# Optimization experiments

Hardware: AMD Instinct MI355X
Metric: run time of the kernel (lower is better)

The kernel has to match this reference:

```python
import jax, jax.numpy as jnp
import numpy as np

B, K, N, D, H, DOUT = 16, 8, 196, 768, 3072, 768


def setup_inputs() -> dict:
    key = jax.random.key(0)
    ks = jax.random.split(key, 5)
    scale_w1 = 1.0 / np.sqrt(D)
    scale_w2 = 1.0 / np.sqrt(H)
    return {
        "slots": jax.random.normal(ks[0], (B, K, D), dtype=jnp.float32),
        "pos_embed": jax.random.normal(ks[1], (N, D), dtype=jnp.float32) * 0.02,
        "map_alpha": jax.random.normal(ks[2], (N, DOUT), dtype=jnp.float32) * 0.02,
        "W1": jax.random.normal(ks[3], (D, H), dtype=jnp.float32) * scale_w1,
        "b1": jnp.zeros((H,), dtype=jnp.float32),
        "W2": jax.random.normal(ks[4], (H, DOUT), dtype=jnp.float32) * scale_w2,
        "b2": jnp.zeros((DOUT,), dtype=jnp.float32),
    }


def reference(slots, pos_embed, map_alpha, W1, b1, W2, b2):
    b, k, d = slots.shape
    n = pos_embed.shape[0]
    # broadcast slots over patches and add positional embedding: (B,K,N,D)
    tokens = slots[:, :, None, :] + pos_embed[None, None, :, :]
    # 2-layer MLP with ReLU
    h = jax.nn.relu(jnp.einsum('bknd,dh->bknh', tokens, W1) + b1)
    y_k = jnp.einsum('bknh,ho->bkno', h, W2) + b2  # (B,K,N,DOUT)
    # softmax over K of map_alpha expanded over (B,K); identical across K -> uniform 1/K,
    # computed explicitly for faithfulness to the original module
    m_k = jax.nn.softmax(jnp.broadcast_to(map_alpha[None, None, :, :], (b, k, n, map_alpha.shape[1])), axis=1)
    y = jnp.einsum('bknd,bknd->bnd', y_k, m_k)
    return y
```

## Files before the change

### kernel.cpp

```cpp
#include <hip/hip_runtime.h>
#include <hip/hip_bf16.h>
#include <stdint.h>


typedef __attribute__((ext_vector_type(8))) short bf16x8;
typedef __attribute__((ext_vector_type(4))) float f32x4;

#define AS1 __attribute__((address_space(1)))
#define AS3 __attribute__((address_space(3)))

#define WAIT_VM(N) asm volatile("s_waitcnt vmcnt(" #N ")" ::: "memory")
#define BAR()      asm volatile("s_barrier" ::: "memory")
#define BAR_LDS()  asm volatile("s_waitcnt lgkmcnt(0)\ns_barrier" ::: "memory")

static __device__ __forceinline__ void gld_lds16(const void* g, void* l) {
    __builtin_amdgcn_global_load_lds((const AS1 unsigned int*)g,
                                     (AS3 unsigned int*)l, 16, 0, 0);
}

static __device__ __forceinline__ unsigned short f2bf(float f) {
    union { float f; unsigned int u; } v; v.f = f;
    unsigned int u = v.u;
    return (unsigned short)((u + 0x7fffu + ((u >> 16) & 1u)) >> 16);
}

static __device__ __forceinline__ void conv_tiled(const float* __restrict__ W,
                                                  unsigned short* __restrict__ Wt,
                                                  int Kd, int Rd, int idx) {
    int r  = idx % Rd;
    int kc = idx / Rd;
    unsigned int po[4];
    #pragma unroll
    for (int j = 0; j < 4; ++j) {
        unsigned short lo = f2bf(W[(size_t)(kc * 8 + 2 * j) * Rd + r]);
        unsigned short hi = f2bf(W[(size_t)(kc * 8 + 2 * j + 1) * Rd + r]);
        po[j] = (unsigned int)lo | ((unsigned int)hi << 16);
    }
    size_t dst = ((size_t)(r >> 6) * (Kd >> 6) + (kc >> 3)) * 4096
               + (size_t)((kc & 7) * 64 + (r & 63)) * 8;
    *(uint4*)(Wt + dst) = make_uint4(po[0], po[1], po[2], po[3]);
}

__global__ void k_prep(const float* __restrict__ W1, unsigned short* __restrict__ W1t,
                       const float* __restrict__ W2, unsigned short* __restrict__ W2t,
                       const float* __restrict__ S, const float* __restrict__ P,
                       unsigned short* __restrict__ A1) {
    int idx = blockIdx.x * blockDim.x + threadIdx.x;
    const int C1n = 96 * 3072;
    const int C2n = 384 * 768;
    const int PKn = 96 * 384;
    if (idx < C1n) {
        conv_tiled(W1, W1t, 768, 3072, idx);
    } else if (idx < C1n + C2n) {
        conv_tiled(W2, W2t, 3072, 768, idx - C1n);
    } else if (idx < C1n + C2n + PKn) {
        int t = idx - C1n - C2n;
        int r  = t % 384;
        int kc = t / 384;
        uint4 o = make_uint4(0u, 0u, 0u, 0u);
        if (r < 324) {
            const float* src = (r < 128) ? (S + (size_t)r * 768 + kc * 8)
                                         : (P + (size_t)(r - 128) * 768 + kc * 8);
            float4 a = *(const float4*)(src);
            float4 b = *(const float4*)(src + 4);
            o.x = (unsigned int)f2bf(a.x) | ((unsigned int)f2bf(a.y) << 16);
            o.y = (unsigned int)f2bf(a.z) | ((unsigned int)f2bf(a.w) << 16);
            o.z = (unsigned int)f2bf(b.x) | ((unsigned int)f2bf(b.y) << 16);
            o.w = (unsigned int)f2bf(b.z) | ((unsigned int)f2bf(b.w) << 16);
        }
        size_t dst = ((size_t)(r >> 6) * 12 + (kc >> 3)) * 4096
                   + (size_t)((kc & 7) * 64 + (r & 63)) * 8;
        *(uint4*)(A1 + dst) = o;
    }
}

__global__ void k_hbar(const float* __restrict__ C1, const float* __restrict__ b1,
                       unsigned short* __restrict__ Hb) {
    const int lane = threadIdx.x & 63;
    const int wv   = threadIdx.x >> 6;
    const int hc   = blockIdx.y * 4 + wv;
    const int h0   = hc * 8;
    const int bn   = blockIdx.x * 64 + lane;
    const int b    = bn / 196;
    const int n    = bn - b * 196;
    const float* prow = C1 + (size_t)(128 + n) * 3072 + h0;
    float4 pA = *(const float4*)(prow);
    float4 pB = *(const float4*)(prow + 4);
    float4 bA = *(const float4*)(b1 + h0);
    float4 bB = *(const float4*)(b1 + h0 + 4);
    float pb[8] = { pA.x + bA.x, pA.y + bA.y, pA.z + bA.z, pA.w + bA.w,
                    pB.x + bB.x, pB.y + bB.y, pB.z + bB.z, pB.w + bB.w };
    float acc[8] = {};
    #pragma unroll
    for (int k = 0; k < 8; ++k) {
        const float* srow = C1 + (size_t)(b * 8 + k) * 3072 + h0;
        float4 sA_ = *(const float4*)(srow);
        float4 sB_ = *(const float4*)(srow + 4);
        acc[0] += fmaxf(sA_.x + pb[0], 0.f);
        acc[1] += fmaxf(sA_.y + pb[1], 0.f);
        acc[2] += fmaxf(sA_.z + pb[2], 0.f);
        acc[3] += fmaxf(sA_.w + pb[3], 0.f);
        acc[4] += fmaxf(sB_.x + pb[4], 0.f);
        acc[5] += fmaxf(sB_.y + pb[5], 0.f);
        acc[6] += fmaxf(sB_.z + pb[6], 0.f);
        acc[7] += fmaxf(sB_.w + pb[7], 0.f);
    }
    unsigned int w0 = (unsigned int)f2bf(acc[0] * 0.125f) | ((unsigned int)f2bf(acc[1] * 0.125f) << 16);
    unsigned int w1 = (unsigned int)f2bf(acc[2] * 0.125f) | ((unsigned int)f2bf(acc[3] * 0.125f) << 16);
    unsigned int w2 = (unsigned int)f2bf(acc[4] * 0.125f) | ((unsigned int)f2bf(acc[5] * 0.125f) << 16);
    unsigned int w3 = (unsigned int)f2bf(acc[6] * 0.125f) | ((unsigned int)f2bf(acc[7] * 0.125f) << 16);
    size_t dst = ((size_t)blockIdx.x * 48 + (hc >> 3)) * 4096
               + (size_t)((hc & 7) * 64 + lane) * 8;
    *(uint4*)(Hb + dst) = make_uint4(w0, w1, w2, w3);
}

__launch_bounds__(256)
__global__ void gemm_tiled(const unsigned short* __restrict__ A,
                           const unsigned short* __restrict__ Bt,
                           const float* __restrict__ bias,
                           float* __restrict__ C,
                           int Mstore, int Nd, int KT) {
    __shared__ unsigned short smem[2 * 8192];

    const int tid  = threadIdx.x;
    const int lane = tid & 63;
    const int wave = tid >> 6;
    const int wm   = wave >> 1;
    const int wn   = wave & 1;
    const int q    = lane >> 4;
    const int l16  = lane & 15;

    const unsigned short* Abase = A  + (size_t)blockIdx.y * KT * 4096;
    const unsigned short* Bbase = Bt + (size_t)blockIdx.x * KT * 4096;

    f32x4 acc[2][2] = {};

    const int offA0 = ((q * 64) + wm * 32 + l16) * 8;
    const int offB0 = ((q * 64) + wn * 32 + l16) * 8;

    {
        #pragma unroll
        for (int it = 0; it < 2; ++it) {
            int c = it * 256 + tid;
            gld_lds16(Abase + (size_t)c * 8, smem + c * 8);
        }
        #pragma unroll
        for (int it = 0; it < 2; ++it) {
            int c = it * 256 + tid;
            gld_lds16(Bbase + (size_t)c * 8, smem + 4096 + c * 8);
        }
    }

    auto step = [&](const unsigned short* sA, const unsigned short* sB,
                    unsigned short* dA, unsigned short* dB, int i) {
        const bool pf = (i + 1 < KT);
        if (pf) {
            const unsigned short* Ag = Abase + (size_t)(i + 1) * 4096;
            const unsigned short* Bg = Bbase + (size_t)(i + 1) * 4096;
            #pragma unroll
            for (int it = 0; it < 2; ++it) {
                int c = it * 256 + tid;
                gld_lds16(Ag + (size_t)c * 8, dA + c * 8);
            }
            #pragma unroll
            for (int it = 0; it < 2; ++it) {
                int c = it * 256 + tid;
                gld_lds16(Bg + (size_t)c * 8, dB + c * 8);
            }
            WAIT_VM(4);
        } else {
            WAIT_VM(0);
        }
        BAR();
        #pragma unroll
        for (int ks = 0; ks < 2; ++ks) {
            const int ko = ks * 4 * 64 * 8;
            bf16x8 af[2], bfr[2];
            af[0]  = *(const bf16x8*)(sA + offA0 + ko);
            af[1]  = *(const bf16x8*)(sA + offA0 + ko + 16 * 8);
            bfr[0] = *(const bf16x8*)(sB + offB0 + ko);
            bfr[1] = *(const bf16x8*)(sB + offB0 + ko + 16 * 8);
            #pragma unroll
            for (int ii = 0; ii < 2; ++ii)
                #pragma unroll
                for (int jj = 0; jj < 2; ++jj)
                    acc[ii][jj] = __builtin_amdgcn_mfma_f32_16x16x32_bf16(
                        af[ii], bfr[jj], acc[ii][jj], 0, 0, 0);
        }
        if (pf) BAR_LDS();
    };

    for (int i = 0; i < KT; i += 2) {
        step(smem,        smem + 4096, smem + 8192, smem + 12288, i);
        step(smem + 8192, smem + 12288, smem,       smem + 4096,  i + 1);
    }

    const int row0 = blockIdx.y * 64 + wm * 32;
    const int col0 = blockIdx.x * 64 + wn * 32;
    #pragma unroll
    for (int ii = 0; ii < 2; ++ii) {
        #pragma unroll
        for (int jj = 0; jj < 2; ++jj) {
            int col = col0 + jj * 16 + l16;
            float bv = bias ? bias[col] : 0.f;
            #pragma unroll
            for (int r = 0; r < 4; ++r) {
                int row = row0 + ii * 16 + q * 4 + r;
                if (row < Mstore) C[(size_t)row * Nd + col] = acc[ii][jj][r] + bv;
            }
        }
    }
}

extern "C" void kernel_launch(void* const* d_in, const int* in_sizes, int n_in,
                              void* d_out, int out_size, void* d_ws, size_t ws_size,
                              hipStream_t stream) {
    const float* slots  = (const float*)d_in[0];
    const float* pos    = (const float*)d_in[1];
    const float* W1     = (const float*)d_in[3];
    const float* b1     = (const float*)d_in[4];
    const float* W2     = (const float*)d_in[5];
    const float* b2     = (const float*)d_in[6];
    float* out = (float*)d_out;

    size_t off = 0;
    auto alloc = [&](size_t bytes) {
        void* p = (char*)d_ws + off;
        off += (bytes + 255) & ~(size_t)255;
        return p;
    };
    unsigned short* W1t = (unsigned short*)alloc((size_t)3072 * 768 * 2);
    unsigned short* W2t = (unsigned short*)alloc((size_t)768 * 3072 * 2);
    unsigned short* A1  = (unsigned short*)alloc((size_t)384 * 768 * 2);
    float*          C1  = (float*)alloc((size_t)324 * 3072 * 4);
    unsigned short* Hb  = (unsigned short*)alloc((size_t)3136 * 3072 * 2);

    const int total = 96 * 3072 + 384 * 768 + 96 * 384;
    k_prep<<<(total + 255) / 256, 256, 0, stream>>>(W1, W1t, W2, W2t, slots, pos, A1);
    gemm_tiled<<<dim3(48, 6), 256, 0, stream>>>(A1, W1t, nullptr, C1, 324, 3072, 12);
    k_hbar<<<dim3(49, 96), 256, 0, stream>>>(C1, b1, Hb);
    gemm_tiled<<<dim3(12, 49), 256, 0, stream>>>(Hb, W2t, b2, out, 3136, 768, 48);
}
```

Baseline: 138.5 us.

## Widen GEMM tile to 64x128 and split-K over two blocks with atomic accumulation

The GEMM kernel now computes a 64x128 output tile per block, with each wave holding a 32x64 accumulator, so each A fragment is reused across more B columns. K is split across two blocks via blockIdx.z, and partial sums are accumulated with float atomicAdd. The prep kernel now zero-fills C1 and pre-initializes the output with b2 so the atomics can accumulate onto it. This trades fewer A loads and better per-wave MFMA density for atomic write traffic, extra initialization writes, and more LDS per block.

```diff
diff --git a/kernel.cpp b/kernel.cpp
--- a/kernel.cpp
+++ b/kernel.cpp
@@ -44,19 +44,22 @@
 __global__ void k_prep(const float* __restrict__ W1, unsigned short* __restrict__ W1t,
                        const float* __restrict__ W2, unsigned short* __restrict__ W2t,
                        const float* __restrict__ S, const float* __restrict__ P,
-                       unsigned short* __restrict__ A1) {
+                       unsigned short* __restrict__ A1,
+                       float* __restrict__ C1, const float* __restrict__ b2,
+                       float* __restrict__ out) {
     int idx = blockIdx.x * blockDim.x + threadIdx.x;
-    const int C1n = 96 * 3072;
-    const int C2n = 384 * 768;
-    const int PKn = 96 * 384;
-    if (idx < C1n) {
-        conv_tiled(W1, W1t, 768, 3072, idx);
-    } else if (idx < C1n + C2n) {
-        conv_tiled(W2, W2t, 3072, 768, idx - C1n);
-    } else if (idx < C1n + C2n + PKn) {
-        int t = idx - C1n - C2n;
-        int r  = t % 384;
-        int kc = t / 384;
+    const int T1 = 96 * 3072;
+    const int T2 = 384 * 768;
+    const int T3 = 96 * 384;
+    const int T4 = 384 * 3072 / 4;
+    const int T5 = 3136 * 768 / 4;
+    if (idx < T1) { conv_tiled(W1, W1t, 768, 3072, idx); return; }
+    idx -= T1;
+    if (idx < T2) { conv_tiled(W2, W2t, 3072, 768, idx); return; }
+    idx -= T2;
+    if (idx < T3) {
+        int r  = idx % 384;
+        int kc = idx / 384;
         uint4 o = make_uint4(0u, 0u, 0u, 0u);
         if (r < 324) {
             const float* src = (r < 128) ? (S + (size_t)r * 768 + kc * 8)
@@ -71,6 +74,15 @@
         size_t dst = ((size_t)(r >> 6) * 12 + (kc >> 3)) * 4096
                    + (size_t)((kc & 7) * 64 + (r & 63)) * 8;
         *(uint4*)(A1 + dst) = o;
+        return;
+    }
+    idx -= T3;
+    if (idx < T4) { *(float4*)(C1 + (size_t)idx * 4) = make_float4(0.f, 0.f, 0.f, 0.f); return; }
+    idx -= T4;
+    if (idx < T5) {
+        int m = idx / 192;
+        int r = idx - m * 192;
+        *(float4*)(out + (size_t)m * 768 + r * 4) = *(const float4*)(b2 + r * 4);
     }
 }
 
@@ -117,10 +129,9 @@
 __launch_bounds__(256)
 __global__ void gemm_tiled(const unsigned short* __restrict__ A,
                            const unsigned short* __restrict__ Bt,
-                           const float* __restrict__ bias,
                            float* __restrict__ C,
-                           int Mstore, int Nd, int KT) {
-    __shared__ unsigned short smem[2 * 8192];
+                           int Mstore, int Nd, int aKT, int bKT, int ktPer) {
+    __shared__ unsigned short smem[2 * 12288];
 
     const int tid  = threadIdx.x;
     const int lane = tid & 63;
@@ -129,84 +140,77 @@
     const int wn   = wave & 1;
     const int q    = lane >> 4;
     const int l16  = lane & 15;
-
-    const unsigned short* Abase = A  + (size_t)blockIdx.y * KT * 4096;
-    const unsigned short* Bbase = Bt + (size_t)blockIdx.x * KT * 4096;
-
-    f32x4 acc[2][2] = {};
-
-    const int offA0 = ((q * 64) + wm * 32 + l16) * 8;
-    const int offB0 = ((q * 64) + wn * 32 + l16) * 8;
-
-    {
-        #pragma unroll
-        for (int it = 0; it < 2; ++it) {
-            int c = it * 256 + tid;
-            gld_lds16(Abase + (size_t)c * 8, smem + c * 8);
-        }
-        #pragma unroll
-        for (int it = 0; it < 2; ++it) {
-            int c = it * 256 + tid;
-            gld_lds16(Bbase + (size_t)c * 8, smem + 4096 + c * 8);
-        }
-    }
-
-    auto step = [&](const unsigned short* sA, const unsigned short* sB,
-                    unsigned short* dA, unsigned short* dB, int i) {
-        const bool pf = (i + 1 < KT);
-        if (pf) {
-            const unsigned short* Ag = Abase + (size_t)(i + 1) * 4096;
-            const unsigned short* Bg = Bbase + (size_t)(i + 1) * 4096;
-            #pragma unroll
-            for (int it = 0; it < 2; ++it) {
-                int c = it * 256 + tid;
-                gld_lds16(Ag + (size_t)c * 8, dA + c * 8);
-            }
-            #pragma unroll
-            for (int it = 0; it < 2; ++it) {
-                int c = it * 256 + tid;
-                gld_lds16(Bg + (size_t)c * 8, dB + c * 8);
-            }
-            WAIT_VM(4);
-        } else {
-            WAIT_VM(0);
-        }
-        BAR();
+    const int nt   = blockIdx.x;
+    const int rt   = blockIdx.y;
+    const int kt0  = blockIdx.z * ktPer;
+
+    const unsigned short* Ab = A  + ((size_t)rt * aKT + kt0) * 4096;
+    const unsigned short* B0 = Bt + ((size_t)(2 * nt)     * bKT + kt0) * 4096;
+    const unsigned short* B1 = Bt + ((size_t)(2 * nt + 1) * bKT + kt0) * 4096;
+
+    f32x4 acc[2][4] = {};
+
+    auto stage = [&](int i, unsigned short* dst) {
+        const unsigned short* Ag  = Ab + (size_t)i * 4096;
+        const unsigned short* Bg0 = B0 + (size_t)i * 4096;
+        const unsigned short* Bg1 = B1 + (size_t)i * 4096;
+        gld_lds16(Ag  + tid * 8,         dst + tid * 8);
+        gld_lds16(Ag  + 2048 + tid * 8,  dst + 2048 + tid * 8);
+        gld_lds16(Bg0 + tid * 8,         dst + 4096 + tid * 8);
+        gld_lds16(Bg0 + 2048 + tid * 8,  dst + 6144 + tid * 8);
+        gld_lds16(Bg1 + tid * 8,         dst + 8192 + tid * 8);
+        gld_lds16(Bg1 + 2048 + tid * 8,  dst + 10240 + tid * 8);
+    };
+
+    const int offA = (wm * 32 + l16) * 8;
+    const int offB = 4096 + wn * 4096 + l16 * 8;
+
+    auto compute = [&](const unsigned short* buf) {
         #pragma unroll
         for (int ks = 0; ks < 2; ++ks) {
-            const int ko = ks * 4 * 64 * 8;
-            bf16x8 af[2], bfr[2];
-            af[0]  = *(const bf16x8*)(sA + offA0 + ko);
-            af[1]  = *(const bf16x8*)(sA + offA0 + ko + 16 * 8);
-            bfr[0] = *(const bf16x8*)(sB + offB0 + ko);
-            bfr[1] = *(const bf16x8*)(sB + offB0 + ko + 16 * 8);
+            const int kb = (ks * 4 + q) * 512;
+            bf16x8 af[2], bfr[4];
+            af[0]  = *(const bf16x8*)(buf + kb + offA);
+            af[1]  = *(const bf16x8*)(buf + kb + offA + 128);
+            const unsigned short* bb = buf + kb + offB;
+            bfr[0] = *(const bf16x8*)(bb);
+            bfr[1] = *(const bf16x8*)(bb + 128);
+            bfr[2] = *(const bf16x8*)(bb + 256);
+            bfr[3] = *(const bf16x8*)(bb + 384);
             #pragma unroll
             for (int ii = 0; ii < 2; ++ii)
                 #pragma unroll
-                for (int jj = 0; jj < 2; ++jj)
+                for (int jj = 0; jj < 4; ++jj)
                     acc[ii][jj] = __builtin_amdgcn_mfma_f32_16x16x32_bf16(
                         af[ii], bfr[jj], acc[ii][jj], 0, 0, 0);
         }
-        if (pf) BAR_LDS();
     };
 
-    for (int i = 0; i < KT; i += 2) {
-        step(smem,        smem + 4096, smem + 8192, smem + 12288, i);
-        step(smem + 8192, smem + 12288, smem,       smem + 4096,  i + 1);
-    }
-
-    const int row0 = blockIdx.y * 64 + wm * 32;
-    const int col0 = blockIdx.x * 64 + wn * 32;
+    stage(0, smem);
+    for (int i = 0; i < ktPer; i += 2) {
+        if (i + 1 < ktPer) { stage(i + 1, smem + 12288); WAIT_VM(6); }
+        else               { WAIT_VM(0); }
+        BAR();
+        compute(smem);
+        BAR_LDS();
+        if (i + 2 < ktPer) { stage(i + 2, smem); WAIT_VM(6); }
+        else               { WAIT_VM(0); }
+        BAR();
+        compute(smem + 12288);
+        if (i + 2 < ktPer) BAR_LDS();
+    }
+
+    const int row0 = rt * 64 + wm * 32;
+    const int col0 = nt * 128 + wn * 64;
     #pragma unroll
     for (int ii = 0; ii < 2; ++ii) {
         #pragma unroll
-        for (int jj = 0; jj < 2; ++jj) {
+        for (int jj = 0; jj < 4; ++jj) {
             int col = col0 + jj * 16 + l16;
-            float bv = bias ? bias[col] : 0.f;
             #pragma unroll
             for (int r = 0; r < 4; ++r) {
                 int row = row0 + ii * 16 + q * 4 + r;
-                if (row < Mstore) C[(size_t)row * Nd + col] = acc[ii][jj][r] + bv;
+                if (row < Mstore) atomicAdd(&C[(size_t)row * Nd + col], acc[ii][jj][r]);
             }
         }
     }
@@ -232,12 +236,11 @@
     unsigned short* W1t = (unsigned short*)alloc((size_t)3072 * 768 * 2);
     unsigned short* W2t = (unsigned short*)alloc((size_t)768 * 3072 * 2);
     unsigned short* A1  = (unsigned short*)alloc((size_t)384 * 768 * 2);
-    float*          C1  = (float*)alloc((size_t)324 * 3072 * 4);
+    float*          C1  = (float*)alloc((size_t)384 * 3072 * 4);
     unsigned short* Hb  = (unsigned short*)alloc((size_t)3136 * 3072 * 2);
 
-    const int total = 96 * 3072 + 384 * 768 + 96 * 384;
-    k_prep<<<(total + 255) / 256, 256, 0, stream>>>(W1, W1t, W2, W2t, slots, pos, A1);
-    gemm_tiled<<<dim3(48, 6), 256, 0, stream>>>(A1, W1t, nullptr, C1, 324, 3072, 12);
+    k_prep<<<5952, 256, 0, stream>>>(W1, W1t, W2, W2t, slots, pos, A1, C1, b2, out);
+    gemm_tiled<<<dim3(24, 6, 2), 256, 0, stream>>>(A1, W1t, C1, 324, 3072, 12, 12, 6);
     k_hbar<<<dim3(49, 96), 256, 0, stream>>>(C1, b1, Hb);
-    gemm_tiled<<<dim3(12, 49), 256, 0, stream>>>(Hb, W2t, b2, out, 3136, 768, 48);
-}
+    gemm_tiled<<<dim3(6, 49, 2), 256, 0, stream>>>(Hb, W2t, out, 3136, 768, 48, 48, 24);
+}
```

Result: slower. 145.5 us (+5.1%).

## Fuse W1/input conversion into first GEMM and deepen second GEMM k-stage

Applied to the files above, without the earlier changes.

Replaces the separate prep kernel and first GEMM with one kernel. It reads fp32 slots, pos and W1 directly, converts them to bf16 into swizzled LDS tiles, and computes the 324x3072 projection with 64x128 tiles. The same launch uses extra blocks to convert W2 into the tiled layout. This removes a launch and the W1t and A1 intermediate round trips through memory. The second GEMM now stages 128-deep K chunks per buffer, which halves barrier count; in exchange the first GEMM does uncoalesced strided W1 loads and no longer double-buffers.

```diff
diff --git a/kernel.cpp b/kernel.cpp
--- a/kernel.cpp
+++ b/kernel.cpp
@@ -24,53 +24,106 @@
     return (unsigned short)((u + 0x7fffu + ((u >> 16) & 1u)) >> 16);
 }
 
-static __device__ __forceinline__ void conv_tiled(const float* __restrict__ W,
-                                                  unsigned short* __restrict__ Wt,
-                                                  int Kd, int Rd, int idx) {
-    int r  = idx % Rd;
-    int kc = idx / Rd;
-    unsigned int po[4];
+static __device__ __forceinline__ uint4 pk8(float4 a, float4 b) {
+    uint4 o;
+    o.x = (unsigned int)f2bf(a.x) | ((unsigned int)f2bf(a.y) << 16);
+    o.y = (unsigned int)f2bf(a.z) | ((unsigned int)f2bf(a.w) << 16);
+    o.z = (unsigned int)f2bf(b.x) | ((unsigned int)f2bf(b.y) << 16);
+    o.w = (unsigned int)f2bf(b.z) | ((unsigned int)f2bf(b.w) << 16);
+    return o;
+}
+
+__launch_bounds__(256)
+__global__ void k_phase1(const float* __restrict__ slots, const float* __restrict__ pos,
+                         const float* __restrict__ W1, float* __restrict__ C1,
+                         const float* __restrict__ W2, unsigned short* __restrict__ W2t) {
+    const int tid = threadIdx.x;
+    const int bx  = blockIdx.x;
+
+    if (bx >= 144) {
+        int idx = (bx - 144) * 256 + tid;
+        int r  = idx % 768;
+        int kc = idx / 768;
+        unsigned int po[4];
+        #pragma unroll
+        for (int j = 0; j < 4; ++j) {
+            unsigned short lo = f2bf(W2[(size_t)(kc * 8 + 2 * j) * 768 + r]);
+            unsigned short hi = f2bf(W2[(size_t)(kc * 8 + 2 * j + 1) * 768 + r]);
+            po[j] = (unsigned int)lo | ((unsigned int)hi << 16);
+        }
+        size_t dst = ((size_t)(r >> 6) * 48 + (kc >> 3)) * 4096
+                   + (size_t)((kc & 7) * 64 + (r & 63)) * 8;
+        *(uint4*)(W2t + dst) = make_uint4(po[0], po[1], po[2], po[3]);
+        return;
+    }
+
+    __shared__ unsigned short sm[12288];
+    const int lane = tid & 63;
+    const int wave = tid >> 6;
+    const int wm = wave >> 1, wn = wave & 1;
+    const int q = lane >> 4, l16 = lane & 15;
+    const int cx = bx % 24, rt = bx / 24;
+    const int col0 = cx * 128;
+
+    f32x4 acc[2][4] = {};
+
+    for (int k0 = 0; k0 < 768; k0 += 64) {
+        __syncthreads();
+        #pragma unroll
+        for (int it = 0; it < 2; ++it) {
+            int c = it * 256 + tid;
+            int m = c & 63, kb = c >> 6;
+            int r = rt * 64 + m; if (r > 323) r = 323;
+            const float* src = (r < 128 ? slots + (size_t)r * 768
+                                        : pos + (size_t)(r - 128) * 768) + k0 + kb * 8;
+            float4 a = *(const float4*)src;
+            float4 b = *(const float4*)(src + 4);
+            *(uint4*)(&sm[m * 64 + ((kb ^ (m & 7)) * 8)]) = pk8(a, b);
+        }
+        #pragma unroll
+        for (int it = 0; it < 4; ++it) {
+            int c = it * 256 + tid;
+            int n = c & 127, kb = c >> 7;
+            const float* src = W1 + (size_t)(k0 + kb * 8) * 3072 + col0 + n;
+            float4 a, b;
+            a.x = src[0];        a.y = src[3072];     a.z = src[2 * 3072]; a.w = src[3 * 3072];
+            b.x = src[4 * 3072]; b.y = src[5 * 3072]; b.z = src[6 * 3072]; b.w = src[7 * 3072];
+            *(uint4*)(&sm[4096 + n * 64 + ((kb ^ (n & 7)) * 8)]) = pk8(a, b);
+        }
+        __syncthreads();
+        #pragma unroll
+        for (int ks = 0; ks < 2; ++ks) {
+            const int kq = ks * 4 + q;
+            bf16x8 af[2], bfr[4];
+            #pragma unroll
+            for (int ii = 0; ii < 2; ++ii) {
+                int m = wm * 32 + ii * 16 + l16;
+                af[ii] = *(const bf16x8*)(&sm[m * 64 + ((kq ^ (m & 7)) * 8)]);
+            }
+            #pragma unroll
+            for (int jj = 0; jj < 4; ++jj) {
+                int n = wn * 64 + jj * 16 + l16;
+                bfr[jj] = *(const bf16x8*)(&sm[4096 + n * 64 + ((kq ^ (n & 7)) * 8)]);
+            }
+            #pragma unroll
+            for (int ii = 0; ii < 2; ++ii)
+                #pragma unroll
+                for (int jj = 0; jj < 4; ++jj)
+                    acc[ii][jj] = __builtin_amdgcn_mfma_f32_16x16x32_bf16(
+                        af[ii], bfr[jj], acc[ii][jj], 0, 0, 0);
+        }
+    }
     #pragma unroll
-    for (int j = 0; j < 4; ++j) {
-        unsigned short lo = f2bf(W[(size_t)(kc * 8 + 2 * j) * Rd + r]);
-        unsigned short hi = f2bf(W[(size_t)(kc * 8 + 2 * j + 1) * Rd + r]);
-        po[j] = (unsigned int)lo | ((unsigned int)hi << 16);
-    }
-    size_t dst = ((size_t)(r >> 6) * (Kd >> 6) + (kc >> 3)) * 4096
-               + (size_t)((kc & 7) * 64 + (r & 63)) * 8;
-    *(uint4*)(Wt + dst) = make_uint4(po[0], po[1], po[2], po[3]);
-}
-
-__global__ void k_prep(const float* __restrict__ W1, unsigned short* __restrict__ W1t,
-                       const float* __restrict__ W2, unsigned short* __restrict__ W2t,
-                       const float* __restrict__ S, const float* __restrict__ P,
-                       unsigned short* __restrict__ A1) {
-    int idx = blockIdx.x * blockDim.x + threadIdx.x;
-    const int C1n = 96 * 3072;
-    const int C2n = 384 * 768;
-    const int PKn = 96 * 384;
-    if (idx < C1n) {
-        conv_tiled(W1, W1t, 768, 3072, idx);
-    } else if (idx < C1n + C2n) {
-        conv_tiled(W2, W2t, 3072, 768, idx - C1n);
-    } else if (idx < C1n + C2n + PKn) {
-        int t = idx - C1n - C2n;
-        int r  = t % 384;
-        int kc = t / 384;
-        uint4 o = make_uint4(0u, 0u, 0u, 0u);
-        if (r < 324) {
-            const float* src = (r < 128) ? (S + (size_t)r * 768 + kc * 8)
-                                         : (P + (size_t)(r - 128) * 768 + kc * 8);
-            float4 a = *(const float4*)(src);
-            float4 b = *(const float4*)(src + 4);
-            o.x = (unsigned int)f2bf(a.x) | ((unsigned int)f2bf(a.y) << 16);
-            o.y = (unsigned int)f2bf(a.z) | ((unsigned int)f2bf(a.w) << 16);
-            o.z = (unsigned int)f2bf(b.x) | ((unsigned int)f2bf(b.y) << 16);
-            o.w = (unsigned int)f2bf(b.z) | ((unsigned int)f2bf(b.w) << 16);
-        }
-        size_t dst = ((size_t)(r >> 6) * 12 + (kc >> 3)) * 4096
-                   + (size_t)((kc & 7) * 64 + (r & 63)) * 8;
-        *(uint4*)(A1 + dst) = o;
+    for (int ii = 0; ii < 2; ++ii) {
+        #pragma unroll
+        for (int jj = 0; jj < 4; ++jj) {
+            int col = col0 + wn * 64 + jj * 16 + l16;
+            #pragma unroll
+            for (int r = 0; r < 4; ++r) {
+                int row = rt * 64 + wm * 32 + ii * 16 + q * 4 + r;
+                if (row < 324) C1[(size_t)row * 3072 + col] = acc[ii][jj][r];
+            }
+        }
     }
 }
 
@@ -115,98 +168,80 @@
 }
 
 __launch_bounds__(256)
-__global__ void gemm_tiled(const unsigned short* __restrict__ A,
-                           const unsigned short* __restrict__ Bt,
-                           const float* __restrict__ bias,
-                           float* __restrict__ C,
-                           int Mstore, int Nd, int KT) {
-    __shared__ unsigned short smem[2 * 8192];
-
+__global__ void k_gemm2(const unsigned short* __restrict__ Hb,
+                        const unsigned short* __restrict__ W2t,
+                        const float* __restrict__ b2, float* __restrict__ out) {
+    __shared__ unsigned short sm[2 * 16384];
     const int tid  = threadIdx.x;
     const int lane = tid & 63;
     const int wave = tid >> 6;
-    const int wm   = wave >> 1;
-    const int wn   = wave & 1;
-    const int q    = lane >> 4;
-    const int l16  = lane & 15;
-
-    const unsigned short* Abase = A  + (size_t)blockIdx.y * KT * 4096;
-    const unsigned short* Bbase = Bt + (size_t)blockIdx.x * KT * 4096;
+    const int wm = wave >> 1, wn = wave & 1;
+    const int q = lane >> 4, l16 = lane & 15;
+    const int nt = blockIdx.x, rt = blockIdx.y;
+
+    const unsigned short* Ab = Hb  + (size_t)rt * 48 * 4096;
+    const unsigned short* Bb = W2t + (size_t)nt * 48 * 4096;
 
     f32x4 acc[2][2] = {};
 
-    const int offA0 = ((q * 64) + wm * 32 + l16) * 8;
-    const int offB0 = ((q * 64) + wn * 32 + l16) * 8;
-
-    {
-        #pragma unroll
-        for (int it = 0; it < 2; ++it) {
-            int c = it * 256 + tid;
-            gld_lds16(Abase + (size_t)c * 8, smem + c * 8);
-        }
-        #pragma unroll
-        for (int it = 0; it < 2; ++it) {
-            int c = it * 256 + tid;
-            gld_lds16(Bbase + (size_t)c * 8, smem + 4096 + c * 8);
-        }
-    }
-
-    auto step = [&](const unsigned short* sA, const unsigned short* sB,
-                    unsigned short* dA, unsigned short* dB, int i) {
-        const bool pf = (i + 1 < KT);
-        if (pf) {
-            const unsigned short* Ag = Abase + (size_t)(i + 1) * 4096;
-            const unsigned short* Bg = Bbase + (size_t)(i + 1) * 4096;
-            #pragma unroll
-            for (int it = 0; it < 2; ++it) {
-                int c = it * 256 + tid;
-                gld_lds16(Ag + (size_t)c * 8, dA + c * 8);
-            }
-            #pragma unroll
-            for (int it = 0; it < 2; ++it) {
-                int c = it * 256 + tid;
-                gld_lds16(Bg + (size_t)c * 8, dB + c * 8);
-            }
-            WAIT_VM(4);
-        } else {
-            WAIT_VM(0);
-        }
+    auto stage = [&](int i, unsigned short* dst) {
+        const unsigned short* Ag = Ab + (size_t)i * 8192;
+        const unsigned short* Bg = Bb + (size_t)i * 8192;
+        #pragma unroll
+        for (int u = 0; u < 4; ++u)
+            gld_lds16(Ag + u * 2048 + tid * 8, dst + u * 2048 + tid * 8);
+        #pragma unroll
+        for (int u = 0; u < 4; ++u)
+            gld_lds16(Bg + u * 2048 + tid * 8, dst + 8192 + u * 2048 + tid * 8);
+    };
+
+    auto compute = [&](const unsigned short* buf) {
+        #pragma unroll
+        for (int a = 0; a < 2; ++a) {
+            #pragma unroll
+            for (int ks = 0; ks < 2; ++ks) {
+                const int kb = a * 4096 + (ks * 4 + q) * 512;
+                bf16x8 af[2], bfr[2];
+                af[0]  = *(const bf16x8*)(buf + kb + (wm * 32 + l16) * 8);
+                af[1]  = *(const bf16x8*)(buf + kb + (wm * 32 + 16 + l16) * 8);
+                bfr[0] = *(const bf16x8*)(buf + 8192 + kb + (wn * 32 + l16) * 8);
+                bfr[1] = *(const bf16x8*)(buf + 8192 + kb + (wn * 32 + 16 + l16) * 8);
+                #pragma unroll
+                for (int ii = 0; ii < 2; ++ii)
+                    #pragma unroll
+                    for (int jj = 0; jj < 2; ++jj)
+                        acc[ii][jj] = __builtin_amdgcn_mfma_f32_16x16x32_bf16(
+                            af[ii], bfr[jj], acc[ii][jj], 0, 0, 0);
+            }
+        }
+    };
+
+    stage(0, sm);
+    for (int i = 0; i < 24; i += 2) {
+        if (i + 1 < 24) { stage(i + 1, sm + 16384); WAIT_VM(8); }
+        else            { WAIT_VM(0); }
         BAR();
-        #pragma unroll
-        for (int ks = 0; ks < 2; ++ks) {
-            const int ko = ks * 4 * 64 * 8;
-            bf16x8 af[2], bfr[2];
-            af[0]  = *(const bf16x8*)(sA + offA0 + ko);
-            af[1]  = *(const bf16x8*)(sA + offA0 + ko + 16 * 8);
-            bfr[0] = *(const bf16x8*)(sB + offB0 + ko);
-            bfr[1] = *(const bf16x8*)(sB + offB0 + ko + 16 * 8);
-            #pragma unroll
-            for (int ii = 0; ii < 2; ++ii)
-                #pragma unroll
-                for (int jj = 0; jj < 2; ++jj)
-                    acc[ii][jj] = __builtin_amdgcn_mfma_f32_16x16x32_bf16(
-                        af[ii], bfr[jj], acc[ii][jj], 0, 0, 0);
-        }
-        if (pf) BAR_LDS();
-    };
-
-    for (int i = 0; i < KT; i += 2) {
-        step(smem,        smem + 4096, smem + 8192, smem + 12288, i);
-        step(smem + 8192, smem + 12288, smem,       smem + 4096,  i + 1);
-    }
-
-    const int row0 = blockIdx.y * 64 + wm * 32;
-    const int col0 = blockIdx.x * 64 + wn * 32;
+        compute(sm);
+        BAR_LDS();
+        if (i + 2 < 24) { stage(i + 2, sm); WAIT_VM(8); }
+        else            { WAIT_VM(0); }
+        BAR();
+        compute(sm + 16384);
+        if (i + 2 < 24) BAR_LDS();
+    }
+
+    const int row0 = rt * 64 + wm * 32;
+    const int col0 = nt * 64 + wn * 32;
     #pragma unroll
     for (int ii = 0; ii < 2; ++ii) {
         #pragma unroll
         for (int jj = 0; jj < 2; ++jj) {
             int col = col0 + jj * 16 + l16;
-            float bv = bias ? bias[col] : 0.f;
+            float bv = b2[col];
             #pragma unroll
             for (int r = 0; r < 4; ++r) {
                 int row = row0 + ii * 16 + q * 4 + r;
-                if (row < Mstore) C[(size_t)row * Nd + col] = acc[ii][jj][r] + bv;
+                out[(size_t)row * 768 + col] = acc[ii][jj][r] + bv;
             }
         }
     }
@@ -229,15 +264,11 @@
         off += (bytes + 255) & ~(size_t)255;
         return p;
     };
-    unsigned short* W1t = (unsigned short*)alloc((size_t)3072 * 768 * 2);
     unsigned short* W2t = (unsigned short*)alloc((size_t)768 * 3072 * 2);
-    unsigned short* A1  = (unsigned short*)alloc((size_t)384 * 768 * 2);
-    float*          C1  = (float*)alloc((size_t)324 * 3072 * 4);
+    float*          C1  = (float*)alloc((size_t)384 * 3072 * 4);
     unsigned short* Hb  = (unsigned short*)alloc((size_t)3136 * 3072 * 2);
 
-    const int total = 96 * 3072 + 384 * 768 + 96 * 384;
-    k_prep<<<(total + 255) / 256, 256, 0, stream>>>(W1, W1t, W2, W2t, slots, pos, A1);
-    gemm_tiled<<<dim3(48, 6), 256, 0, stream>>>(A1, W1t, nullptr, C1, 324, 3072, 12);
+    k_phase1<<<1296, 256, 0, stream>>>(slots, pos, W1, C1, W2, W2t);
     k_hbar<<<dim3(49, 96), 256, 0, stream>>>(C1, b1, Hb);
-    gemm_tiled<<<dim3(12, 49), 256, 0, stream>>>(Hb, W2t, b2, out, 3136, 768, 48);
-}
+    k_gemm2<<<dim3(12, 49), 256, 0, stream>>>(Hb, W2t, b2, out);
+}
```

Measured after the change: 159.4 us. 1.15x slower.
